# Optimization experiments

Measured on AMD Instinct MI355X. Metric: run time of the kernel, lower is better.

Reference implementation:

```python
import jax, jax.numpy as jnp
import numpy as np

N_NODES = 500_000
N_EDGES = 8_000_000
N_GRAPHS = 1000


def _mlp(x, w1, b1, w2, b2):
    # Linear -> SELU -> Linear (torch Sequential equivalent)
    return jax.nn.selu(x @ w1 + b1) @ w2 + b2


def setup_inputs() -> dict:
    key = jax.random.key(0)
    ks = jax.random.split(key, 25)
    p = lambda i, shape: jax.random.normal(ks[i], shape, jnp.float32) * 0.1
    return {
        "nodes": jax.random.normal(ks[0], (N_NODES, 1), jnp.float32),
        "edges": jax.random.normal(ks[1], (N_EDGES, 1), jnp.float32),
        "senders": jax.random.randint(ks[2], (N_EDGES,), 0, N_NODES),
        "receivers": jax.random.randint(ks[3], (N_EDGES,), 0, N_NODES),
        "graph_ids": jnp.sort(jax.random.randint(ks[4], (N_NODES,), 0, N_GRAPHS)),
        "num_graphs": N_GRAPHS,
        # permutate_nodes: 2 -> 10 -> 10
        "pn_w1": p(5, (2, 10)), "pn_b1": p(6, (10,)), "pn_w2": p(7, (10, 10)), "pn_b2": p(8, (10,)),
        # update_edges: 11 -> 5 -> 1
        "ue_w1": p(9, (11, 5)), "ue_b1": p(10, (5,)), "ue_w2": p(11, (5, 1)), "ue_b2": p(12, (1,)),
        # permutate_edges: 1 -> 5 -> 10
        "pe_w1": p(13, (1, 5)), "pe_b1": p(14, (5,)), "pe_w2": p(15, (5, 10)), "pe_b2": p(16, (10,)),
        # update_nodes: 11 -> 5 -> 1
        "un_w1": p(17, (11, 5)), "un_b1": p(18, (5,)), "un_w2": p(19, (5, 1)), "un_b2": p(20, (1,)),
        # predict: 11 -> 10 -> 10
        "pr_w1": p(21, (11, 10)), "pr_b1": p(22, (10,)), "pr_w2": p(23, (10, 10)), "pr_b2": p(24, (10,)),
    }


def reference(nodes, edges, pn_w1, pn_b1, pn_w2, pn_b2,
              ue_w1, ue_b1, ue_w2, ue_b2,
              pe_w1, pe_b1, pe_w2, pe_b2,
              un_w1, un_b1, un_w2, un_b2,
              pr_w1, pr_b1, pr_w2, pr_b2,
              senders, receivers, graph_ids, num_graphs):
    # gather node feats to edges: [recv || send] -> (E, 2)
    collected = jnp.concatenate([nodes[receivers], nodes[senders]], axis=-1)
    h1_nodes = _mlp(collected, pn_w1, pn_b1, pn_w2, pn_b2)  # (E, 10)
    h1_edges = edges  # (E, 1)
    for _ in range(3):
        h1_edges = _mlp(jnp.concatenate([h1_edges, h1_nodes], axis=-1),
                        ue_w1, ue_b1, ue_w2, ue_b2)  # (E, 1)
    # edges -> nodes aggregation (sum over receiver)
    edges_of_nodes = jax.ops.segment_sum(h1_edges, receivers, num_segments=nodes.shape[0])  # (N, 1)
    h2_edges = _mlp(edges_of_nodes, pe_w1, pe_b1, pe_w2, pe_b2)  # (N, 10)
    h2_nodes = nodes  # (N, 1)
    for _ in range(3):
        h2_nodes = _mlp(jnp.concatenate([h2_nodes, h2_edges], axis=-1),
                        un_w1, un_b1, un_w2, un_b2)  # (N, 1)
    # nodes -> globals aggregation (sum per graph)
    g = jax.ops.segment_sum(jnp.concatenate([h2_nodes, h2_edges], axis=-1),
                            graph_ids, num_segments=num_graphs)  # (G, 11)
    out = _mlp(g, pr_w1, pr_b1, pr_w2, pr_b2)  # (G, 10)
    return jax.nn.softmax(out, axis=-1)
```

## Files before the change

### kernel.cpp

```cpp
#include <hip/hip_runtime.h>
#include <hip/hip_fp16.h>
#include <math.h>

#define N_NODES_C  500000
#define N_EDGES_C  8000000
#define N_GRAPHS_C 1000
#define NGROUPS_C  (N_EDGES_C / 4)

#define BSHIFT  11
#define BWIDTH  2048
#define NBKT    245
#define PART_TPB 512
#define EPB     16384
#define GPB     (EPB / 4)
#define NPB     ((NGROUPS_C + GPB - 1) / GPB)
#define SROW    496
#define RITER   (GPB / PART_TPB)

#define G_BSHIFT 10
#define G_BWIDTH 1024
#define G_NBKT   489
#define P3_TPB  512
#define EPB3    8192
#define GPB3    (EPB3 / 4)
#define NPB3    ((NGROUPS_C + GPB3 - 1) / GPB3)
#define RITER3  (GPB3 / P3_TPB)

#define GRAPH_ACC_OFF 0
#define PARTIALS_OFF  11008
#define FW_OFF        33024
#define ZERO_HEAD     33024

#define STARTS_OFF    33280
#define PAIRS_OFF     (STARTS_OFF + 246 * SROW)
#define WS_WORDS_NEEDED (PAIRS_OFF + NPB * EPB)

#define GTOT_OFF   33248
#define GCUR_OFF   33760
#define RPFX_OFF   34272
#define PAIRS3_OFF 34784
#define WS3_WORDS_NEEDED (PAIRS3_OFF + N_EDGES_C * 2)

#define OLD_NODE_ACC_OFF 33536
#define OLD_ZERO_WORDS   (OLD_NODE_ACC_OFF + N_NODES_C)

#define LOG2E_F 1.4426950408889634f


__device__ __forceinline__ float selu2(float xl) {
    const float C1 = 0.7282901039f;
    const float C2 = 1.7580993408473766f;
    float e = __builtin_amdgcn_exp2f(xl);
    float neg = fmaf(C2, e, -C2);
    return xl > 0.0f ? C1 * xl : neg;
}

__device__ __forceinline__ float selu_f(float x) {
    const float scale = 1.0507009873554805f;
    const float sa    = 1.0507009873554805f * 1.6732632423543772f;
    float neg = sa * (__expf(x) - 1.0f);
    return x > 0.0f ? scale * x : neg;
}

__device__ __forceinline__ void atomAddF(float* p, float v) {
    __hip_atomic_fetch_add(p, v, __ATOMIC_RELAXED, __HIP_MEMORY_SCOPE_AGENT);
}

__device__ __forceinline__ void fuse_weights(
        int t,
        const float* __restrict__ pn_w1, const float* __restrict__ pn_b1,
        const float* __restrict__ pn_w2, const float* __restrict__ pn_b2,
        const float* __restrict__ ue_w1, const float* __restrict__ ue_b1,
        const float* __restrict__ ue_w2, const float* __restrict__ ue_b2,
        const float* __restrict__ pe_w1, const float* __restrict__ pe_b1,
        const float* __restrict__ pe_w2, const float* __restrict__ pe_b2,
        const float* __restrict__ un_w1, const float* __restrict__ un_b1,
        const float* __restrict__ un_w2, const float* __restrict__ un_b2,
        float* __restrict__ fw) {
    const float L = LOG2E_F;
    if (t < 20) fw[0 + t] = pn_w1[t] * L;
    if (t < 10) fw[20 + t] = pn_b1[t] * L;
    if (t < 50) {
        int j = t / 5, k = t % 5;
        float s = 0.0f;
        for (int m = 0; m < 10; ++m) s += pn_w2[j * 10 + m] * ue_w1[(1 + m) * 5 + k];
        fw[30 + t] = s * L;
    }
    if (t < 5) {
        float s = ue_b1[t];
        for (int m = 0; m < 10; ++m) s += pn_b2[m] * ue_w1[(1 + m) * 5 + t];
        fw[80 + t] = s * L;
    }
    if (t < 5)  fw[85 + t]  = ue_w1[t] * L;
    if (t < 5)  fw[90 + t]  = ue_w2[t];
    if (t == 0) fw[95]      = ue_b2[0];
    if (t < 5)  fw[96 + t]  = pe_w1[t] * L;
    if (t < 5)  fw[101 + t] = pe_b1[t] * L;
    if (t < 50) fw[106 + t] = pe_w2[t];
    if (t < 10) fw[156 + t] = pe_b2[t];
    if (t < 25) {
        int j = t / 5, k = t % 5;
        float s = 0.0f;
        for (int m = 0; m < 10; ++m) s += pe_w2[j * 10 + m] * un_w1[(1 + m) * 5 + k];
        fw[166 + t] = s * L;
    }
    if (t < 5) {
        float s = un_b1[t];
        for (int m = 0; m < 10; ++m) s += pe_b2[m] * un_w1[(1 + m) * 5 + t];
        fw[191 + t] = s * L;
    }
    if (t < 5)  fw[196 + t] = un_w1[t] * L;
    if (t < 5)  fw[201 + t] = un_w2[t];
    if (t == 0) fw[206]     = un_b2[0];
}

__global__ __launch_bounds__(256) void k_init(
        float* __restrict__ ws,
        const float* pn_w1, const float* pn_b1, const float* pn_w2, const float* pn_b2,
        const float* ue_w1, const float* ue_b1, const float* ue_w2, const float* ue_b2,
        const float* pe_w1, const float* pe_b1, const float* pe_w2, const float* pe_b2,
        const float* un_w1, const float* un_b1, const float* un_w2, const float* un_b2) {
    int i = blockIdx.x * 256 + threadIdx.x;
    if (i < ZERO_HEAD) ws[i] = 0.0f;
    int* gtot = (int*)ws + GTOT_OFF;
    if (i < 512) gtot[i] = 0;
    if (blockIdx.x == 0)
        fuse_weights(threadIdx.x, pn_w1, pn_b1, pn_w2, pn_b2, ue_w1, ue_b1, ue_w2, ue_b2,
                     pe_w1, pe_b1, pe_w2, pe_b2, un_w1, un_b1, un_w2, un_b2, ws + FW_OFF);
}

__global__ void k_fuse(const float* pn_w1, const float* pn_b1, const float* pn_w2, const float* pn_b2,
                       const float* ue_w1, const float* ue_b1, const float* ue_w2, const float* ue_b2,
                       const float* pe_w1, const float* pe_b1, const float* pe_w2, const float* pe_b2,
                       const float* un_w1, const float* un_b1, const float* un_w2, const float* un_b2,
                       float* fw) {
    fuse_weights(threadIdx.x, pn_w1, pn_b1, pn_w2, pn_b2, ue_w1, ue_b1, ue_w2, ue_b2,
                 pe_w1, pe_b1, pe_w2, pe_b2, un_w1, un_b1, un_w2, un_b2, fw);
}

__global__ void k_final(const float* __restrict__ graph_acc,
                        const float* __restrict__ partials,
                        const float* __restrict__ pr_w1, const float* __restrict__ pr_b1,
                        const float* __restrict__ pr_w2, const float* __restrict__ pr_b2,
                        float* __restrict__ out) {
    int g = blockIdx.x * blockDim.x + threadIdx.x;
    if (g >= N_GRAPHS_C) return;
    float gv[11];
#pragma unroll
    for (int f = 0; f < 11; ++f)
        gv[f] = graph_acc[g * 11 + f] + partials[g * 11 + f] + partials[11000 + g * 11 + f];
    float h[10];
#pragma unroll
    for (int j = 0; j < 10; ++j) {
        float z = pr_b1[j];
#pragma unroll
        for (int f = 0; f < 11; ++f) z = fmaf(gv[f], pr_w1[f * 10 + j], z);
        h[j] = selu_f(z);
    }
    float o[10];
    float mx = -1e30f;
#pragma unroll
    for (int j = 0; j < 10; ++j) {
        float z = pr_b2[j];
#pragma unroll
        for (int m = 0; m < 10; ++m) z = fmaf(h[m], pr_w2[m * 10 + j], z);
        o[j] = z;
        mx = fmaxf(mx, z);
    }
    float sum = 0.0f;
#pragma unroll
    for (int j = 0; j < 10; ++j) { o[j] = __expf(o[j] - mx); sum += o[j]; }
    float inv = 1.0f / sum;
#pragma unroll
    for (int j = 0; j < 10; ++j) out[g * 10 + j] = o[j] * inv;
}


__global__ __launch_bounds__(P3_TPB) void k_hist(
        const int* __restrict__ receivers, int* __restrict__ gtot) {
    __shared__ int hist[512];
    int tid = threadIdx.x, p = blockIdx.x;
    int gstart = p * GPB3;
    int gnum   = NGROUPS_C - gstart;
    if (gnum > GPB3) gnum = GPB3;
    hist[tid] = 0;
    __syncthreads();
#pragma unroll
    for (int r = 0; r < RITER3; ++r) {
        int idx = r * P3_TPB + tid;
        int gi  = gstart + (idx < gnum ? idx : 0);
        int4 rv = ((const int4*)receivers)[gi];
        if (idx < gnum) {
            atomicAdd(&hist[rv.x >> G_BSHIFT], 1);
            atomicAdd(&hist[rv.y >> G_BSHIFT], 1);
            atomicAdd(&hist[rv.z >> G_BSHIFT], 1);
            atomicAdd(&hist[rv.w >> G_BSHIFT], 1);
        }
    }
    __syncthreads();
    int h = hist[tid];
    if (h) atomicAdd(&gtot[tid], h);
}

__global__ __launch_bounds__(512) void k_rowscan(
        const int* __restrict__ gtot, int* __restrict__ gcursor,
        int* __restrict__ rowprefix) {
    __shared__ int sc[512];
    int tid = threadIdx.x;
    int v = (tid < G_NBKT) ? gtot[tid] : 0;
    sc[tid] = v;
    __syncthreads();
    int val = v;
    for (int d = 1; d < 512; d <<= 1) {
        int add = (tid >= d) ? sc[tid - d] : 0;
        __syncthreads();
        if (tid >= d) { val += add; sc[tid] = val; }
        __syncthreads();
    }
    int excl = val - v;
    gcursor[tid]  = excl;
    rowprefix[tid] = excl;
    if (tid == G_NBKT - 1) rowprefix[G_NBKT] = val;
}

__global__ __launch_bounds__(P3_TPB, 4) void k_part3(
        const float* __restrict__ edges,
        const int* __restrict__ senders, const int* __restrict__ receivers,
        int* __restrict__ gcursor, unsigned long long* __restrict__ pairs64) {
    __shared__ int hist[512];
    __shared__ int cursor[512];
    __shared__ int lstartS[512];
    __shared__ int segbase[512];
    __shared__ alignas(16) unsigned long long staged[EPB3];

    int tid = threadIdx.x, p = blockIdx.x;
    int gstart = p * GPB3;
    int gnum   = NGROUPS_C - gstart;
    if (gnum > GPB3) gnum = GPB3;
    int E = gnum * 4;

    hist[tid] = 0;
    __syncthreads();

    int4 rv4[RITER3];
#pragma unroll
    for (int r = 0; r < RITER3; ++r) {
        int idx = r * P3_TPB + tid;
        int gi  = gstart + (idx < gnum ? idx : 0);
        rv4[r] = ((const int4*)receivers)[gi];
        if (idx < gnum) {
            atomicAdd(&hist[rv4[r].x >> G_BSHIFT], 1);
            atomicAdd(&hist[rv4[r].y >> G_BSHIFT], 1);
            atomicAdd(&hist[rv4[r].z >> G_BSHIFT], 1);
            atomicAdd(&hist[rv4[r].w >> G_BSHIFT], 1);
        }
    }
    __syncthreads();

    int orig = hist[tid], val = orig;
    for (int d = 1; d < 512; d <<= 1) {
        int add = (tid >= d) ? hist[tid - d] : 0;
        __syncthreads();
        if (tid >= d) { val += add; hist[tid] = val; }
        __syncthreads();
    }
    int excl = val - orig;
    cursor[tid]  = excl;
    lstartS[tid] = excl;
    __syncthreads();

    if (tid < G_NBKT) {
        int cnt = ((tid + 1 < 512) ? lstartS[tid + 1] : E) - excl;
        segbase[tid] = atomicAdd(&gcursor[tid], cnt);
    }

#pragma unroll
    for (int r = 0; r < RITER3; ++r) {
        int idx = r * P3_TPB + tid;
        int gi  = gstart + (idx < gnum ? idx : 0);
        float4 e4 = ((const float4*)edges)[gi];
        int4   s4 = ((const int4*)senders)[gi];
        int4   rv = rv4[r];
        if (idx < gnum) {
            int   rvv[4] = {rv.x, rv.y, rv.z, rv.w};
            int   svv[4] = {s4.x, s4.y, s4.z, s4.w};
            float evv[4] = {e4.x, e4.y, e4.z, e4.w};
#pragma unroll
            for (int u = 0; u < 4; ++u) {
                int bkt  = rvv[u] >> G_BSHIFT;
                int slot = atomicAdd(&cursor[bkt], 1);
                unsigned long long pk =
                    ((unsigned long long)(rvv[u] & (G_BWIDTH - 1)) << 51)
                  | ((unsigned long long)(unsigned)svv[u] << 32)
                  | (unsigned long long)__float_as_uint(evv[u]);
                staged[slot] = pk;
            }
        }
    }
    __syncthreads();

#pragma unroll 2
    for (int i = tid; i < E; i += P3_TPB) {
        int lo = 0, hi = 512;
#pragma unroll
        for (int s = 0; s < 9; ++s) {
            int mid = (lo + hi) >> 1;
            if (lstartS[mid] <= i) lo = mid; else hi = mid;
        }
        pairs64[(size_t)segbase[lo] + (i - lstartS[lo])] = staged[i];
    }
}

__global__ __launch_bounds__(1024, 8) void k_gather3(
        const float* __restrict__ nodes, const int* __restrict__ graph_ids,
        const float* __restrict__ fw, const int* __restrict__ rowprefix,
        const unsigned long long* __restrict__ pairs64,
        float* __restrict__ graph_acc, float* __restrict__ partials) {
    __shared__ float accf[G_BWIDTH];
    __shared__ float nf[G_BWIDTH];
    __shared__ float garr[32 * 11];
    int tid = threadIdx.x;
    int b   = blockIdx.x;

    int nodeBase = b << G_BSHIFT;
    int lastIdx  = nodeBase + G_BWIDTH;
    if (lastIdx > N_NODES_C) lastIdx = N_NODES_C;
    int lim = lastIdx - nodeBase;

    accf[tid] = 0.0f;
    nf[tid]   = (tid < lim) ? nodes[nodeBase + tid] : 0.0f;
    if (tid < 352) garr[tid] = 0.0f;
    int base = rowprefix[b];
    int end  = rowprefix[b + 1];
    __syncthreads();

    {
        float w_pn1[20], b_pn1[10], W_eb[50], b_eb[5], w1r0[5], w2e[5];
#pragma unroll
        for (int j = 0; j < 20; ++j) w_pn1[j] = fw[j];
#pragma unroll
        for (int j = 0; j < 10; ++j) b_pn1[j] = fw[20 + j];
#pragma unroll
        for (int j = 0; j < 50; ++j) W_eb[j] = fw[30 + j];
#pragma unroll
        for (int j = 0; j < 5; ++j) b_eb[j] = fw[80 + j];
#pragma unroll
        for (int j = 0; j < 5; ++j) w1r0[j] = fw[85 + j];
#pragma unroll
        for (int j = 0; j < 5; ++j) w2e[j] = fw[90 + j];
        float b2e = fw[95];

        int i = base + tid;
#pragma unroll 1
        for (; i + 1024 < end; i += 2048) {
            unsigned long long pkA = pairs64[i];
            unsigned long long pkB = pairs64[i + 1024];
            float nsA = nodes[(int)((pkA >> 32) & 0x7FFFFULL)];
            float nsB = nodes[(int)((pkB >> 32) & 0x7FFFFULL)];
            int   rlA = (int)(pkA >> 51);
            int   rlB = (int)(pkB >> 51);
            float nrA = nf[rlA];
            float nrB = nf[rlB];
            float eA  = __uint_as_float((unsigned)pkA);
            float eB  = __uint_as_float((unsigned)pkB);

            float bsA[5], bsB[5];
#pragma unroll
            for (int k = 0; k < 5; ++k) { bsA[k] = b_eb[k]; bsB[k] = b_eb[k]; }
#pragma unroll
            for (int j = 0; j < 10; ++j) {
                float zlA = fmaf(nrA, w_pn1[j], fmaf(nsA, w_pn1[10 + j], b_pn1[j]));
                float zlB = fmaf(nrB, w_pn1[j], fmaf(nsB, w_pn1[10 + j], b_pn1[j]));
                float szA = selu2(zlA);
                float szB = selu2(zlB);
#pragma unroll
                for (int k = 0; k < 5; ++k) {
                    bsA[k] = fmaf(szA, W_eb[j * 5 + k], bsA[k]);
                    bsB[k] = fmaf(szB, W_eb[j * 5 + k], bsB[k]);
                }
            }
#pragma unroll
            for (int it = 0; it < 3; ++it) {
                float aA = b2e, aB = b2e;
#pragma unroll
                for (int k = 0; k < 5; ++k) {
                    float tA = selu2(fmaf(eA, w1r0[k], bsA[k]));
                    float tB = selu2(fmaf(eB, w1r0[k], bsB[k]));
                    aA = fmaf(tA, w2e[k], aA);
                    aB = fmaf(tB, w2e[k], aB);
                }
                eA = aA; eB = aB;
            }
            atomicAdd(&accf[rlA], eA);
            atomicAdd(&accf[rlB], eB);
        }
#pragma unroll 1
        for (; i < end; i += 1024) {
            unsigned long long pk = pairs64[i];
            int   rl   = (int)(pk >> 51);
            int   sidx = (int)((pk >> 32) & 0x7FFFFULL);
            float e    = __uint_as_float((unsigned)pk);
            float nr   = nf[rl];
            float ns   = nodes[sidx];

            float bs[5];
#pragma unroll
            for (int k = 0; k < 5; ++k) bs[k] = b_eb[k];
#pragma unroll
            for (int j = 0; j < 10; ++j) {
                float zl = fmaf(nr, w_pn1[j], fmaf(ns, w_pn1[10 + j], b_pn1[j]));
                float sz = selu2(zl);
#pragma unroll
                for (int k = 0; k < 5; ++k) bs[k] = fmaf(sz, W_eb[j * 5 + k], bs[k]);
            }
#pragma unroll
            for (int it = 0; it < 3; ++it) {
                float acc2 = b2e;
#pragma unroll
                for (int k = 0; k < 5; ++k) {
                    float tt = selu2(fmaf(e, w1r0[k], bs[k]));
                    acc2 = fmaf(tt, w2e[k], acc2);
                }
                e = acc2;
            }
            atomicAdd(&accf[rl], e);
        }
    }
    __syncthreads();

    float w_pe1[5], b_pe1[5], pe_w2[50], pe_b2[10], W_nb[25], b_nb[5], w1r0n[5], w2n[5];
#pragma unroll
    for (int j = 0; j < 5; ++j) w_pe1[j] = fw[96 + j];
#pragma unroll
    for (int j = 0; j < 5; ++j) b_pe1[j] = fw[101 + j];
#pragma unroll
    for (int j = 0; j < 50; ++j) pe_w2[j] = fw[106 + j];
#pragma unroll
    for (int j = 0; j < 10; ++j) pe_b2[j] = fw[156 + j];
#pragma unroll
    for (int j = 0; j < 25; ++j) W_nb[j] = fw[166 + j];
#pragma unroll
    for (int j = 0; j < 5; ++j) b_nb[j] = fw[191 + j];
#pragma unroll
    for (int j = 0; j < 5; ++j) w1r0n[j] = fw[196 + j];
#pragma unroll
    for (int j = 0; j < 5; ++j) w2n[j] = fw[201 + j];
    float b2n = fw[206];

    int gidBase = graph_ids[nodeBase];
    int gidEnd  = graph_ids[lastIdx - 1];

    {
        int i = nodeBase + tid;
        bool valid = tid < lim;

        float s = accf[tid];
        float t5[5];
#pragma unroll
        for (int k = 0; k < 5; ++k) t5[k] = selu2(fmaf(s, w_pe1[k], b_pe1[k]));
        float he[10];
#pragma unroll
        for (int m = 0; m < 10; ++m) {
            float a = pe_b2[m];
#pragma unroll
            for (int k = 0; k < 5; ++k) a = fmaf(t5[k], pe_w2[k * 10 + m], a);
            he[m] = a;
        }
        float bs[5];
#pragma unroll
        for (int k = 0; k < 5; ++k) {
            float a = b_nb[k];
#pragma unroll
            for (int t = 0; t < 5; ++t) a = fmaf(t5[t], W_nb[t * 5 + k], a);
            bs[k] = a;
        }
        float n = valid ? nf[tid] : 0.0f;
#pragma unroll
        for (int it = 0; it < 3; ++it) {
            float a = b2n;
#pragma unroll
            for (int k = 0; k < 5; ++k) {
                float tt = selu2(fmaf(n, w1r0n[k], bs[k]));
                a = fmaf(tt, w2n[k], a);
            }
            n = a;
        }

        int gid = valid ? graph_ids[i] : -1;
        if (!valid) {
            n = 0.0f;
#pragma unroll
            for (int m = 0; m < 10; ++m) he[m] = 0.0f;
        }

        int gid0 = __shfl(gid, 0, 64);
        bool allsame = __all(gid == gid0) && (gid0 >= 0);
        if (allsame) {
            float vv = n;
#pragma unroll
            for (int off = 32; off > 0; off >>= 1) vv += __shfl_down(vv, off, 64);
            float vh[10];
#pragma unroll
            for (int m = 0; m < 10; ++m) {
                float ww = he[m];
#pragma unroll
                for (int off = 32; off > 0; off >>= 1) ww += __shfl_down(ww, off, 64);
                vh[m] = ww;
            }
            if ((tid & 63) == 0) {
                int off = gid0 - gidBase;
                if (off >= 0 && off < 32) {
                    atomicAdd(&garr[off * 11 + 0], vv);
#pragma unroll
                    for (int m = 0; m < 10; ++m) atomicAdd(&garr[off * 11 + 1 + m], vh[m]);
                } else {
                    atomAddF(&graph_acc[gid0 * 11 + 0], vv);
#pragma unroll
                    for (int m = 0; m < 10; ++m) atomAddF(&graph_acc[gid0 * 11 + 1 + m], vh[m]);
                }
            }
        } else if (valid) {
            int off = gid - gidBase;
            if (off >= 0 && off < 32) {
                atomicAdd(&garr[off * 11 + 0], n);
#pragma unroll
                for (int m = 0; m < 10; ++m) atomicAdd(&garr[off * 11 + 1 + m], he[m]);
            } else {
                atomAddF(&graph_acc[gid * 11 + 0], n);
#pragma unroll
                for (int m = 0; m < 10; ++m) atomAddF(&graph_acc[gid * 11 + 1 + m], he[m]);
            }
        }
    }
    __syncthreads();

    int ngl = gidEnd - gidBase + 1;
    if (ngl > 32) ngl = 32;
    int par = (b & 1) * 11000;
    for (int t = tid; t < ngl * 11; t += 1024) {
        int off = t / 11, f = t - off * 11;
        partials[par + (gidBase + off) * 11 + f] = garr[t];
    }
}


__global__ __launch_bounds__(PART_TPB, 4) void k_part(
        const float* __restrict__ nodes, const float* __restrict__ edges,
        const int* __restrict__ senders, const int* __restrict__ receivers,
        const float* __restrict__ fw, int* __restrict__ starts_T,
        unsigned int* __restrict__ pairs) {
    __shared__ int hist[256];
    __shared__ int cursorS[256];
    __shared__ unsigned int staged[EPB];

    int tid = threadIdx.x;
    int p   = blockIdx.x;
    int gstart = p * GPB;
    int gnum   = NGROUPS_C - gstart;
    if (gnum > GPB) gnum = GPB;

    float w_pn1[20], b_pn1[10], W_eb[50], b_eb[5], w1r0[5], w2e[5];
#pragma unroll
    for (int j = 0; j < 20; ++j) w_pn1[j] = fw[j];
#pragma unroll
    for (int j = 0; j < 10; ++j) b_pn1[j] = fw[20 + j];
#pragma unroll
    for (int j = 0; j < 50; ++j) W_eb[j] = fw[30 + j];
#pragma unroll
    for (int j = 0; j < 5; ++j) b_eb[j] = fw[80 + j];
#pragma unroll
    for (int j = 0; j < 5; ++j) w1r0[j] = fw[85 + j];
#pragma unroll
    for (int j = 0; j < 5; ++j) w2e[j] = fw[90 + j];
    float b2e = fw[95];

    if (tid < 256) hist[tid] = 0;
    __syncthreads();

#pragma unroll 1
    for (int r = 0; r < RITER; ++r) {
        int idx = r * PART_TPB + tid;
        int gi  = gstart + (idx < gnum ? idx : 0);
        int4 rv = ((const int4*)receivers)[gi];
        if (idx < gnum) {
            atomicAdd(&hist[rv.x >> BSHIFT], 1);
            atomicAdd(&hist[rv.y >> BSHIFT], 1);
            atomicAdd(&hist[rv.z >> BSHIFT], 1);
            atomicAdd(&hist[rv.w >> BSHIFT], 1);
        }
    }
    __syncthreads();

    int orig = 0, val = 0;
    if (tid < 256) { orig = hist[tid]; val = orig; }
    for (int d = 1; d < 256; d <<= 1) {
        int add = 0;
        if (tid >= d && tid < 256) add = hist[tid - d];
        __syncthreads();
        if (tid >= d && tid < 256) { val += add; hist[tid] = val; }
        __syncthreads();
    }
    int excl = val - orig;
    if (tid < 256) cursorS[tid] = excl;
    if (tid < 246) starts_T[tid * SROW + p] = excl;
    __syncthreads();

    float4 e4A, e4B, e4N;
    int4   s4A, s4B, s4N, r4A, r4B, r4N;
    float  nsA0, nsA1, nsA2, nsA3, nrA0, nrA1, nrA2, nrA3;
    float  nsB0, nsB1, nsB2, nsB3, nrB0, nrB1, nrB2, nrB3;

    {
        int gi0 = gstart + (tid < gnum ? tid : 0);
        e4A = ((const float4*)edges)[gi0];
        s4A = ((const int4*)senders)[gi0];
        r4A = ((const int4*)receivers)[gi0];
        nsA0 = nodes[s4A.x]; nsA1 = nodes[s4A.y];
        nsA2 = nodes[s4A.z]; nsA3 = nodes[s4A.w];
        nrA0 = nodes[r4A.x]; nrA1 = nodes[r4A.y];
        nrA2 = nodes[r4A.z]; nrA3 = nodes[r4A.w];
        int idx1 = PART_TPB + tid;
        int gi1 = gstart + (idx1 < gnum ? idx1 : 0);
        e4B = ((const float4*)edges)[gi1];
        s4B = ((const int4*)senders)[gi1];
        r4B = ((const int4*)receivers)[gi1];
    }

#pragma unroll 1
    for (int r = 0; r < RITER; ++r) {
        {
            int idx2 = (r + 2) * PART_TPB + tid;
            int gi2  = gstart + (idx2 < gnum ? idx2 : 0);
            e4N = ((const float4*)edges)[gi2];
            s4N = ((const int4*)senders)[gi2];
            r4N = ((const int4*)receivers)[gi2];
        }
        nsB0 = nodes[s4B.x]; nsB1 = nodes[s4B.y];
        nsB2 = nodes[s4B.z]; nsB3 = nodes[s4B.w];
        nrB0 = nodes[r4B.x]; nrB1 = nodes[r4B.y];
        nrB2 = nodes[r4B.z]; nrB3 = nodes[r4B.w];

        float ev[4]  = {e4A.x, e4A.y, e4A.z, e4A.w};
        int   rv[4]  = {r4A.x, r4A.y, r4A.z, r4A.w};
        float nsv[4] = {nsA0, nsA1, nsA2, nsA3};
        float nrv[4] = {nrA0, nrA1, nrA2, nrA3};

        bool validr = (r * PART_TPB + tid) < gnum;
#pragma unroll
        for (int u = 0; u < 4; ++u) {
            float nr = nrv[u], ns = nsv[u];
            float bs[5];
#pragma unroll
            for (int k = 0; k < 5; ++k) bs[k] = b_eb[k];
#pragma unroll
            for (int j = 0; j < 10; ++j) {
                float zl = fmaf(nr, w_pn1[j], fmaf(ns, w_pn1[10 + j], b_pn1[j]));
                float sz = selu2(zl);
#pragma unroll
                for (int k = 0; k < 5; ++k) bs[k] = fmaf(sz, W_eb[j * 5 + k], bs[k]);
            }
            float e = ev[u];
#pragma unroll
            for (int it = 0; it < 3; ++it) {
                float acc2 = b2e;
#pragma unroll
                for (int k = 0; k < 5; ++k) {
                    float tt = selu2(fmaf(e, w1r0[k], bs[k]));
                    acc2 = fmaf(tt, w2e[k], acc2);
                }
                e = acc2;
            }
            if (validr) {
                int bkt  = rv[u] >> BSHIFT;
                int slot = atomicAdd(&cursorS[bkt], 1);
                unsigned int pk = ((unsigned int)(rv[u] & (BWIDTH - 1)) << 16)
                                | (unsigned int)__half_as_ushort(__float2half_rn(e));
                staged[slot] = pk;
            }
        }

        e4A = e4B; s4A = s4B; r4A = r4B;
        nsA0 = nsB0; nsA1 = nsB1; nsA2 = nsB2; nsA3 = nsB3;
        nrA0 = nrB0; nrA1 = nrB1; nrA2 = nrB2; nrA3 = nrB3;
        e4B = e4N; s4B = s4N; r4B = r4N;
    }
    __syncthreads();

    const uint4* staged4 = (const uint4*)staged;
    uint4* dst = (uint4*)(pairs + (size_t)p * EPB);
    for (int i = tid; i < gnum; i += PART_TPB) dst[i] = staged4[i];
}

__global__ __launch_bounds__(1024) void k_gather(
        const float* __restrict__ nodes, const int* __restrict__ graph_ids,
        const float* __restrict__ fw, const int* __restrict__ starts_T,
        const unsigned int* __restrict__ pairs, float* __restrict__ graph_acc,
        float* __restrict__ partials) {
    __shared__ float accf[BWIDTH];
    __shared__ int s0[SROW], s1[SROW];
    __shared__ float garr[32 * 11];
    int tid = threadIdx.x;
    int b   = blockIdx.x;

    accf[tid] = 0.0f; accf[1024 + tid] = 0.0f;
    if (tid < 352) garr[tid] = 0.0f;
    for (int i = tid; i < NPB; i += 1024) {
        s0[i] = starts_T[b * SROW + i];
        s1[i] = starts_T[(b + 1) * SROW + i];
    }
    __syncthreads();

    int g32 = tid >> 5, lane = tid & 31;
    for (int p = g32; p < NPB; p += 32) {
        int st = s0[p], en = s1[p];
        const unsigned int* seg = pairs + (size_t)p * EPB + st;
        int cnt = en - st;
        for (int i = lane; i < cnt; i += 32) {
            unsigned int pk = seg[i];
            atomicAdd(&accf[(pk >> 16) & (BWIDTH - 1)],
                      __half2float(__ushort_as_half((unsigned short)(pk & 0xffff))));
        }
    }
    __syncthreads();

    float w_pe1[5], b_pe1[5], pe_w2[50], pe_b2[10], W_nb[25], b_nb[5], w1r0n[5], w2n[5];
#pragma unroll
    for (int j = 0; j < 5; ++j) w_pe1[j] = fw[96 + j];
#pragma unroll
    for (int j = 0; j < 5; ++j) b_pe1[j] = fw[101 + j];
#pragma unroll
    for (int j = 0; j < 50; ++j) pe_w2[j] = fw[106 + j];
#pragma unroll
    for (int j = 0; j < 10; ++j) pe_b2[j] = fw[156 + j];
#pragma unroll
    for (int j = 0; j < 25; ++j) W_nb[j] = fw[166 + j];
#pragma unroll
    for (int j = 0; j < 5; ++j) b_nb[j] = fw[191 + j];
#pragma unroll
    for (int j = 0; j < 5; ++j) w1r0n[j] = fw[196 + j];
#pragma unroll
    for (int j = 0; j < 5; ++j) w2n[j] = fw[201 + j];
    float b2n = fw[206];

    int nodeBase = b << BSHIFT;
    int lastIdx  = nodeBase + BWIDTH;
    if (lastIdx > N_NODES_C) lastIdx = N_NODES_C;
    int gidBase = graph_ids[nodeBase];
    int gidEnd  = graph_ids[lastIdx - 1];

#pragma unroll
    for (int q = 0; q < 2; ++q) {
        int local = q * 1024 + tid;
        int i = nodeBase + local;
        bool valid = i < N_NODES_C;

        float s = accf[local];
        float t5[5];
#pragma unroll
        for (int k = 0; k < 5; ++k) t5[k] = selu2(fmaf(s, w_pe1[k], b_pe1[k]));
        float he[10];
#pragma unroll
        for (int m = 0; m < 10; ++m) {
            float a = pe_b2[m];
#pragma unroll
            for (int k = 0; k < 5; ++k) a = fmaf(t5[k], pe_w2[k * 10 + m], a);
            he[m] = a;
        }
        float bs[5];
#pragma unroll
        for (int k = 0; k < 5; ++k) {
            float a = b_nb[k];
#pragma unroll
            for (int t = 0; t < 5; ++t) a = fmaf(t5[t], W_nb[t * 5 + k], a);
            bs[k] = a;
        }
        float n = valid ? nodes[i] : 0.0f;
#pragma unroll
        for (int it = 0; it < 3; ++it) {
            float a = b2n;
#pragma unroll
            for (int k = 0; k < 5; ++k) {
                float tt = selu2(fmaf(n, w1r0n[k], bs[k]));
                a = fmaf(tt, w2n[k], a);
            }
            n = a;
        }

        int gid = valid ? graph_ids[i] : -1;
        if (!valid) {
            n = 0.0f;
#pragma unroll
            for (int m = 0; m < 10; ++m) he[m] = 0.0f;
        }

        int gid0 = __shfl(gid, 0, 64);
        bool allsame = __all(gid == gid0) && (gid0 >= 0);
        if (allsame) {
            float v = n;
#pragma unroll
            for (int off = 32; off > 0; off >>= 1) v += __shfl_down(v, off, 64);
            float vh[10];
#pragma unroll
            for (int m = 0; m < 10; ++m) {
                float ww = he[m];
#pragma unroll
                for (int off = 32; off > 0; off >>= 1) ww += __shfl_down(ww, off, 64);
                vh[m] = ww;
            }
            if ((tid & 63) == 0) {
                int off = gid0 - gidBase;
                if (off >= 0 && off < 32) {
                    atomicAdd(&garr[off * 11 + 0], v);
#pragma unroll
                    for (int m = 0; m < 10; ++m) atomicAdd(&garr[off * 11 + 1 + m], vh[m]);
                } else {
                    atomAddF(&graph_acc[gid0 * 11 + 0], v);
#pragma unroll
                    for (int m = 0; m < 10; ++m) atomAddF(&graph_acc[gid0 * 11 + 1 + m], vh[m]);
                }
            }
        } else if (valid) {
            int off = gid - gidBase;
            if (off >= 0 && off < 32) {
                atomicAdd(&garr[off * 11 + 0], n);
#pragma unroll
                for (int m = 0; m < 10; ++m) atomicAdd(&garr[off * 11 + 1 + m], he[m]);
            } else {
                atomAddF(&graph_acc[gid * 11 + 0], n);
#pragma unroll
                for (int m = 0; m < 10; ++m) atomAddF(&graph_acc[gid * 11 + 1 + m], he[m]);
            }
        }
    }
    __syncthreads();

    int ngl = gidEnd - gidBase + 1;
    if (ngl > 32) ngl = 32;
    int par = (b & 1) * 11000;
    for (int t = tid; t < ngl * 11; t += 1024) {
        int off = t / 11, f = t - off * 11;
        partials[par + (gidBase + off) * 11 + f] = garr[t];
    }
}


__global__ __launch_bounds__(256) void k_zero(float* __restrict__ ws, int len4) {
    int i = blockIdx.x * 256 + threadIdx.x;
    if (i < len4) ((float4*)ws)[i] = make_float4(0.f, 0.f, 0.f, 0.f);
}

__global__ __launch_bounds__(256) void k_edges(
        const float* __restrict__ nodes, const float* __restrict__ edges,
        const int* __restrict__ senders, const int* __restrict__ receivers,
        const float* __restrict__ fw, float* __restrict__ node_acc) {
    float w_pn1[20], b_pn1[10], W_eb[50], b_eb[5], w1r0[5], w2e[5];
#pragma unroll
    for (int j = 0; j < 20; ++j) w_pn1[j] = fw[j];
#pragma unroll
    for (int j = 0; j < 10; ++j) b_pn1[j] = fw[20 + j];
#pragma unroll
    for (int j = 0; j < 50; ++j) W_eb[j] = fw[30 + j];
#pragma unroll
    for (int j = 0; j < 5; ++j) b_eb[j] = fw[80 + j];
#pragma unroll
    for (int j = 0; j < 5; ++j) w1r0[j] = fw[85 + j];
#pragma unroll
    for (int j = 0; j < 5; ++j) w2e[j] = fw[90 + j];
    float b2e = fw[95];

    int g = blockIdx.x * 256 + threadIdx.x;
    if (g >= NGROUPS_C) return;

    float4 e4 = ((const float4*)edges)[g];
    int4  s4 = ((const int4*)senders)[g];
    int4  r4 = ((const int4*)receivers)[g];
    float ev[4] = {e4.x, e4.y, e4.z, e4.w};
    int   sv[4] = {s4.x, s4.y, s4.z, s4.w};
    int   rv[4] = {r4.x, r4.y, r4.z, r4.w};
    float nsv[4], nrv[4];
#pragma unroll
    for (int u = 0; u < 4; ++u) { nsv[u] = nodes[sv[u]]; nrv[u] = nodes[rv[u]]; }
#pragma unroll
    for (int u = 0; u < 4; ++u) {
        float nr = nrv[u], ns = nsv[u];
        float bs[5];
#pragma unroll
        for (int k = 0; k < 5; ++k) bs[k] = b_eb[k];
#pragma unroll
        for (int j = 0; j < 10; ++j) {
            float zl = fmaf(nr, w_pn1[j], fmaf(ns, w_pn1[10 + j], b_pn1[j]));
            float sz = selu2(zl);
#pragma unroll
            for (int k = 0; k < 5; ++k) bs[k] = fmaf(sz, W_eb[j * 5 + k], bs[k]);
        }
        float e = ev[u];
#pragma unroll
        for (int it = 0; it < 3; ++it) {
            float acc2 = b2e;
#pragma unroll
            for (int k = 0; k < 5; ++k) {
                float tt = selu2(fmaf(e, w1r0[k], bs[k]));
                acc2 = fmaf(tt, w2e[k], acc2);
            }
            e = acc2;
        }
        atomAddF(&node_acc[rv[u]], e);
    }
}

__global__ __launch_bounds__(256) void k_nodes(
        const float* __restrict__ nodes, const int* __restrict__ graph_ids,
        const float* __restrict__ fw, const float* __restrict__ node_acc,
        float* __restrict__ graph_acc) {
    float w_pe1[5], b_pe1[5], pe_w2[50], pe_b2[10], W_nb[25], b_nb[5], w1r0n[5], w2n[5];
#pragma unroll
    for (int j = 0; j < 5; ++j) w_pe1[j] = fw[96 + j];
#pragma unroll
    for (int j = 0; j < 5; ++j) b_pe1[j] = fw[101 + j];
#pragma unroll
    for (int j = 0; j < 50; ++j) pe_w2[j] = fw[106 + j];
#pragma unroll
    for (int j = 0; j < 10; ++j) pe_b2[j] = fw[156 + j];
#pragma unroll
    for (int j = 0; j < 25; ++j) W_nb[j] = fw[166 + j];
#pragma unroll
    for (int j = 0; j < 5; ++j) b_nb[j] = fw[191 + j];
#pragma unroll
    for (int j = 0; j < 5; ++j) w1r0n[j] = fw[196 + j];
#pragma unroll
    for (int j = 0; j < 5; ++j) w2n[j] = fw[201 + j];
    float b2n = fw[206];

    int i = blockIdx.x * 256 + threadIdx.x;
    bool valid = i < N_NODES_C;
    int ii = valid ? i : (N_NODES_C - 1);

    float s = node_acc[ii];
    float t5[5];
#pragma unroll
    for (int k = 0; k < 5; ++k) t5[k] = selu2(fmaf(s, w_pe1[k], b_pe1[k]));
    float he[10];
#pragma unroll
    for (int m = 0; m < 10; ++m) {
        float a = pe_b2[m];
#pragma unroll
        for (int k = 0; k < 5; ++k) a = fmaf(t5[k], pe_w2[k * 10 + m], a);
        he[m] = a;
    }
    float bs[5];
#pragma unroll
    for (int k = 0; k < 5; ++k) {
        float a = b_nb[k];
#pragma unroll
        for (int t = 0; t < 5; ++t) a = fmaf(t5[t], W_nb[t * 5 + k], a);
        bs[k] = a;
    }
    float n = nodes[ii];
#pragma unroll
    for (int it = 0; it < 3; ++it) {
        float a = b2n;
#pragma unroll
        for (int k = 0; k < 5; ++k) {
            float tt = selu2(fmaf(n, w1r0n[k], bs[k]));
            a = fmaf(tt, w2n[k], a);
        }
        n = a;
    }

    int gid = valid ? graph_ids[ii] : -1;
    if (!valid) {
        n = 0.0f;
#pragma unroll
        for (int m = 0; m < 10; ++m) he[m] = 0.0f;
    }

    int gid0 = __shfl(gid, 0, 64);
    bool allsame = __all(gid == gid0) && (gid0 >= 0);
    if (allsame) {
        float v = n;
#pragma unroll
        for (int off = 32; off > 0; off >>= 1) v += __shfl_down(v, off, 64);
        float vh[10];
#pragma unroll
        for (int m = 0; m < 10; ++m) {
            float ww = he[m];
#pragma unroll
            for (int off = 32; off > 0; off >>= 1) ww += __shfl_down(ww, off, 64);
            vh[m] = ww;
        }
        if ((threadIdx.x & 63) == 0) {
            atomAddF(&graph_acc[gid0 * 11 + 0], v);
#pragma unroll
            for (int m = 0; m < 10; ++m) atomAddF(&graph_acc[gid0 * 11 + 1 + m], vh[m]);
        }
    } else if (valid) {
        atomAddF(&graph_acc[gid * 11 + 0], n);
#pragma unroll
        for (int m = 0; m < 10; ++m) atomAddF(&graph_acc[gid * 11 + 1 + m], he[m]);
    }
}


extern "C" void kernel_launch(void* const* d_in, const int* in_sizes, int n_in,
                              void* d_out, int out_size, void* d_ws, size_t ws_size,
                              hipStream_t stream) {
    const float* nodes     = (const float*)d_in[0];
    const float* edges     = (const float*)d_in[1];
    const int*   senders   = (const int*)d_in[2];
    const int*   receivers = (const int*)d_in[3];
    const int*   graph_ids = (const int*)d_in[4];
    const float* pn_w1 = (const float*)d_in[6];
    const float* pn_b1 = (const float*)d_in[7];
    const float* pn_w2 = (const float*)d_in[8];
    const float* pn_b2 = (const float*)d_in[9];
    const float* ue_w1 = (const float*)d_in[10];
    const float* ue_b1 = (const float*)d_in[11];
    const float* ue_w2 = (const float*)d_in[12];
    const float* ue_b2 = (const float*)d_in[13];
    const float* pe_w1 = (const float*)d_in[14];
    const float* pe_b1 = (const float*)d_in[15];
    const float* pe_w2 = (const float*)d_in[16];
    const float* pe_b2 = (const float*)d_in[17];
    const float* un_w1 = (const float*)d_in[18];
    const float* un_b1 = (const float*)d_in[19];
    const float* un_w2 = (const float*)d_in[20];
    const float* un_b2 = (const float*)d_in[21];
    const float* pr_w1 = (const float*)d_in[22];
    const float* pr_b1 = (const float*)d_in[23];
    const float* pr_w2 = (const float*)d_in[24];
    const float* pr_b2 = (const float*)d_in[25];

    float* ws        = (float*)d_ws;
    float* graph_acc = ws + GRAPH_ACC_OFF;
    float* partials  = ws + PARTIALS_OFF;
    float* fw        = ws + FW_OFF;
    float* outp      = (float*)d_out;

    if (ws_size >= (size_t)WS3_WORDS_NEEDED * 4) {
        int* gtot      = (int*)ws + GTOT_OFF;
        int* gcursor   = (int*)ws + GCUR_OFF;
        int* rowprefix = (int*)ws + RPFX_OFF;
        unsigned long long* pairs64 = (unsigned long long*)((int*)ws + PAIRS3_OFF);

        hipLaunchKernelGGL(k_init, dim3((ZERO_HEAD + 255) / 256), dim3(256), 0, stream, ws,
                           pn_w1, pn_b1, pn_w2, pn_b2, ue_w1, ue_b1, ue_w2, ue_b2,
                           pe_w1, pe_b1, pe_w2, pe_b2, un_w1, un_b1, un_w2, un_b2);
        hipLaunchKernelGGL(k_hist, dim3(NPB3), dim3(P3_TPB), 0, stream,
                           receivers, gtot);
        hipLaunchKernelGGL(k_rowscan, dim3(1), dim3(512), 0, stream,
                           gtot, gcursor, rowprefix);
        hipLaunchKernelGGL(k_part3, dim3(NPB3), dim3(P3_TPB), 0, stream,
                           edges, senders, receivers, gcursor, pairs64);
        hipLaunchKernelGGL(k_gather3, dim3(G_NBKT), dim3(1024), 0, stream,
                           nodes, graph_ids, fw, rowprefix, pairs64, graph_acc, partials);
        hipLaunchKernelGGL(k_final, dim3((N_GRAPHS_C + 255) / 256), dim3(256), 0, stream,
                           graph_acc, partials, pr_w1, pr_b1, pr_w2, pr_b2, outp);
    } else if (ws_size >= (size_t)WS_WORDS_NEEDED * 4) {
        int* starts_T        = (int*)ws + STARTS_OFF;
        unsigned int* pairs  = (unsigned int*)ws + PAIRS_OFF;

        hipLaunchKernelGGL(k_init, dim3((ZERO_HEAD + 255) / 256), dim3(256), 0, stream, ws,
                           pn_w1, pn_b1, pn_w2, pn_b2, ue_w1, ue_b1, ue_w2, ue_b2,
                           pe_w1, pe_b1, pe_w2, pe_b2, un_w1, un_b1, un_w2, un_b2);
        hipLaunchKernelGGL(k_part, dim3(NPB), dim3(PART_TPB), 0, stream,
                           nodes, edges, senders, receivers, fw, starts_T, pairs);
        hipLaunchKernelGGL(k_gather, dim3(NBKT), dim3(1024), 0, stream,
                           nodes, graph_ids, fw, starts_T, pairs, graph_acc, partials);
        hipLaunchKernelGGL(k_final, dim3((N_GRAPHS_C + 255) / 256), dim3(256), 0, stream,
                           graph_acc, partials, pr_w1, pr_b1, pr_w2, pr_b2, outp);
    } else {
        float* node_acc = ws + OLD_NODE_ACC_OFF;
        int len4 = OLD_ZERO_WORDS / 4;
        hipLaunchKernelGGL(k_zero, dim3((len4 + 255) / 256), dim3(256), 0, stream, ws, len4);
        hipLaunchKernelGGL(k_fuse, dim3(1), dim3(64), 0, stream,
                           pn_w1, pn_b1, pn_w2, pn_b2, ue_w1, ue_b1, ue_w2, ue_b2,
                           pe_w1, pe_b1, pe_w2, pe_b2, un_w1, un_b1, un_w2, un_b2, fw);
        hipLaunchKernelGGL(k_edges, dim3((NGROUPS_C + 255) / 256), dim3(256), 0, stream,
                           nodes, edges, senders, receivers, fw, node_acc);
        hipLaunchKernelGGL(k_nodes, dim3((N_NODES_C + 255) / 256), dim3(256), 0, stream,
                           nodes, graph_ids, fw, node_acc, graph_acc);
        hipLaunchKernelGGL(k_final, dim3((N_GRAPHS_C + 255) / 256), dim3(256), 0, stream,
                           graph_acc, partials, pr_w1, pr_b1, pr_w2, pr_b2, outp);
    }
}
```

Before: 338.0 us.

## Pre-gather sender node values in partition pass and pack edges as fp16

The partition kernel now loads senders early, gathers nodes[sender] there, and packs that float value into the 64-bit pair along with an fp16 edge value and a 16-bit local receiver index. The gather kernel no longer does a dependent random load of nodes. The init work is fused into the histogram kernel, with gtot cleared by a memset. Nontemporal loads and stores are used for the streaming data, and the part3 occupancy hint is lowered. Rounding the edge feature to fp16 adds numerical error.

Result: slower. 372.7 us (+10.2%).

```diff
diff --git a/kernel.cpp b/kernel.cpp
--- a/kernel.cpp
+++ b/kernel.cpp
@@ -45,6 +45,9 @@
 #define OLD_ZERO_WORDS   (OLD_NODE_ACC_OFF + N_NODES_C)
 
 #define LOG2E_F 1.4426950408889634f
+
+typedef int   int4v __attribute__((ext_vector_type(4)));
+typedef float flt4v __attribute__((ext_vector_type(4)));
 
 
 __device__ __forceinline__ float selu2(float xl) {
@@ -122,8 +125,6 @@
         const float* un_w1, const float* un_b1, const float* un_w2, const float* un_b2) {
     int i = blockIdx.x * 256 + threadIdx.x;
     if (i < ZERO_HEAD) ws[i] = 0.0f;
-    int* gtot = (int*)ws + GTOT_OFF;
-    if (i < 512) gtot[i] = 0;
     if (blockIdx.x == 0)
         fuse_weights(threadIdx.x, pn_w1, pn_b1, pn_w2, pn_b2, ue_w1, ue_b1, ue_w2, ue_b2,
                      pe_w1, pe_b1, pe_w2, pe_b2, un_w1, un_b1, un_w2, un_b2, ws + FW_OFF);
@@ -176,10 +177,21 @@
 }
 
 
-__global__ __launch_bounds__(P3_TPB) void k_hist(
-        const int* __restrict__ receivers, int* __restrict__ gtot) {
+__global__ __launch_bounds__(P3_TPB) void k_inithist(
+        float* __restrict__ ws, const int* __restrict__ receivers,
+        int* __restrict__ gtot,
+        const float* pn_w1, const float* pn_b1, const float* pn_w2, const float* pn_b2,
+        const float* ue_w1, const float* ue_b1, const float* ue_w2, const float* ue_b2,
+        const float* pe_w1, const float* pe_b1, const float* pe_w2, const float* pe_b2,
+        const float* un_w1, const float* un_b1, const float* un_w2, const float* un_b2) {
     __shared__ int hist[512];
     int tid = threadIdx.x, p = blockIdx.x;
+    int gt = p * P3_TPB + tid;
+    if (gt < ZERO_HEAD) ws[gt] = 0.0f;
+    if (p == 0)
+        fuse_weights(tid, pn_w1, pn_b1, pn_w2, pn_b2, ue_w1, ue_b1, ue_w2, ue_b2,
+                     pe_w1, pe_b1, pe_w2, pe_b2, un_w1, un_b1, un_w2, un_b2, ws + FW_OFF);
+
     int gstart = p * GPB3;
     int gnum   = NGROUPS_C - gstart;
     if (gnum > GPB3) gnum = GPB3;
@@ -189,12 +201,12 @@
     for (int r = 0; r < RITER3; ++r) {
         int idx = r * P3_TPB + tid;
         int gi  = gstart + (idx < gnum ? idx : 0);
-        int4 rv = ((const int4*)receivers)[gi];
+        int4v rv = __builtin_nontemporal_load((const int4v*)receivers + gi);
         if (idx < gnum) {
-            atomicAdd(&hist[rv.x >> G_BSHIFT], 1);
-            atomicAdd(&hist[rv.y >> G_BSHIFT], 1);
-            atomicAdd(&hist[rv.z >> G_BSHIFT], 1);
-            atomicAdd(&hist[rv.w >> G_BSHIFT], 1);
+            atomicAdd(&hist[rv[0] >> G_BSHIFT], 1);
+            atomicAdd(&hist[rv[1] >> G_BSHIFT], 1);
+            atomicAdd(&hist[rv[2] >> G_BSHIFT], 1);
+            atomicAdd(&hist[rv[3] >> G_BSHIFT], 1);
         }
     }
     __syncthreads();
@@ -223,8 +235,8 @@
     if (tid == G_NBKT - 1) rowprefix[G_NBKT] = val;
 }
 
-__global__ __launch_bounds__(P3_TPB, 4) void k_part3(
-        const float* __restrict__ edges,
+__global__ __launch_bounds__(P3_TPB, 2) void k_part3(
+        const float* __restrict__ nodes, const float* __restrict__ edges,
         const int* __restrict__ senders, const int* __restrict__ receivers,
         int* __restrict__ gcursor, unsigned long long* __restrict__ pairs64) {
     __shared__ int hist[512];
@@ -242,17 +254,19 @@
     hist[tid] = 0;
     __syncthreads();
 
-    int4 rv4[RITER3];
+    int4v rv4[RITER3];
+    int4v s4v[RITER3];
 #pragma unroll
     for (int r = 0; r < RITER3; ++r) {
         int idx = r * P3_TPB + tid;
         int gi  = gstart + (idx < gnum ? idx : 0);
-        rv4[r] = ((const int4*)receivers)[gi];
+        rv4[r] = __builtin_nontemporal_load((const int4v*)receivers + gi);
+        s4v[r] = __builtin_nontemporal_load((const int4v*)senders + gi);
         if (idx < gnum) {
-            atomicAdd(&hist[rv4[r].x >> G_BSHIFT], 1);
-            atomicAdd(&hist[rv4[r].y >> G_BSHIFT], 1);
-            atomicAdd(&hist[rv4[r].z >> G_BSHIFT], 1);
-            atomicAdd(&hist[rv4[r].w >> G_BSHIFT], 1);
+            atomicAdd(&hist[rv4[r][0] >> G_BSHIFT], 1);
+            atomicAdd(&hist[rv4[r][1] >> G_BSHIFT], 1);
+            atomicAdd(&hist[rv4[r][2] >> G_BSHIFT], 1);
+            atomicAdd(&hist[rv4[r][3] >> G_BSHIFT], 1);
         }
     }
     __syncthreads();
@@ -274,25 +288,30 @@
         segbase[tid] = atomicAdd(&gcursor[tid], cnt);
     }
 
+    float nsv[RITER3][4];
+#pragma unroll
+    for (int r = 0; r < RITER3; ++r) {
+        nsv[r][0] = nodes[s4v[r][0]];
+        nsv[r][1] = nodes[s4v[r][1]];
+        nsv[r][2] = nodes[s4v[r][2]];
+        nsv[r][3] = nodes[s4v[r][3]];
+    }
+
 #pragma unroll
     for (int r = 0; r < RITER3; ++r) {
         int idx = r * P3_TPB + tid;
         int gi  = gstart + (idx < gnum ? idx : 0);
-        float4 e4 = ((const float4*)edges)[gi];
-        int4   s4 = ((const int4*)senders)[gi];
-        int4   rv = rv4[r];
+        flt4v e4 = __builtin_nontemporal_load((const flt4v*)edges + gi);
         if (idx < gnum) {
-            int   rvv[4] = {rv.x, rv.y, rv.z, rv.w};
-            int   svv[4] = {s4.x, s4.y, s4.z, s4.w};
-            float evv[4] = {e4.x, e4.y, e4.z, e4.w};
 #pragma unroll
             for (int u = 0; u < 4; ++u) {
-                int bkt  = rvv[u] >> G_BSHIFT;
+                int rv   = rv4[r][u];
+                int bkt  = rv >> G_BSHIFT;
                 int slot = atomicAdd(&cursor[bkt], 1);
                 unsigned long long pk =
-                    ((unsigned long long)(rvv[u] & (G_BWIDTH - 1)) << 51)
-                  | ((unsigned long long)(unsigned)svv[u] << 32)
-                  | (unsigned long long)__float_as_uint(evv[u]);
+                    ((unsigned long long)(rv & (G_BWIDTH - 1)) << 48)
+                  | ((unsigned long long)__half_as_ushort(__float2half_rn(e4[u])) << 32)
+                  | (unsigned long long)__float_as_uint(nsv[r][u]);
                 staged[slot] = pk;
             }
         }
@@ -307,7 +326,8 @@
             int mid = (lo + hi) >> 1;
             if (lstartS[mid] <= i) lo = mid; else hi = mid;
         }
-        pairs64[(size_t)segbase[lo] + (i - lstartS[lo])] = staged[i];
+        __builtin_nontemporal_store(
+            staged[i], &pairs64[(size_t)segbase[lo] + (i - lstartS[lo])]);
     }
 }
 
@@ -353,16 +373,16 @@
         int i = base + tid;
 #pragma unroll 1
         for (; i + 1024 < end; i += 2048) {
-            unsigned long long pkA = pairs64[i];
-            unsigned long long pkB = pairs64[i + 1024];
-            float nsA = nodes[(int)((pkA >> 32) & 0x7FFFFULL)];
-            float nsB = nodes[(int)((pkB >> 32) & 0x7FFFFULL)];
-            int   rlA = (int)(pkA >> 51);
-            int   rlB = (int)(pkB >> 51);
+            unsigned long long pkA = __builtin_nontemporal_load(&pairs64[i]);
+            unsigned long long pkB = __builtin_nontemporal_load(&pairs64[i + 1024]);
+            int   rlA = (int)(pkA >> 48);
+            int   rlB = (int)(pkB >> 48);
+            float eA  = __half2float(__ushort_as_half((unsigned short)(pkA >> 32)));
+            float eB  = __half2float(__ushort_as_half((unsigned short)(pkB >> 32)));
+            float nsA = __uint_as_float((unsigned)pkA);
+            float nsB = __uint_as_float((unsigned)pkB);
             float nrA = nf[rlA];
             float nrB = nf[rlB];
-            float eA  = __uint_as_float((unsigned)pkA);
-            float eB  = __uint_as_float((unsigned)pkB);
 
             float bsA[5], bsB[5];
 #pragma unroll
@@ -396,12 +416,11 @@
         }
 #pragma unroll 1
         for (; i < end; i += 1024) {
-            unsigned long long pk = pairs64[i];
-            int   rl   = (int)(pk >> 51);
-            int   sidx = (int)((pk >> 32) & 0x7FFFFULL);
-            float e    = __uint_as_float((unsigned)pk);
-            float nr   = nf[rl];
-            float ns   = nodes[sidx];
+            unsigned long long pk = __builtin_nontemporal_load(&pairs64[i]);
+            int   rl = (int)(pk >> 48);
+            float e  = __half2float(__ushort_as_half((unsigned short)(pk >> 32)));
+            float ns = __uint_as_float((unsigned)pk);
+            float nr = nf[rl];
 
             float bs[5];
 #pragma unroll
@@ -1042,15 +1061,15 @@
         int* rowprefix = (int*)ws + RPFX_OFF;
         unsigned long long* pairs64 = (unsigned long long*)((int*)ws + PAIRS3_OFF);
 
-        hipLaunchKernelGGL(k_init, dim3((ZERO_HEAD + 255) / 256), dim3(256), 0, stream, ws,
+        hipMemsetAsync(gtot, 0, 512 * sizeof(int), stream);
+        hipLaunchKernelGGL(k_inithist, dim3(NPB3), dim3(P3_TPB), 0, stream,
+                           ws, receivers, gtot,
                            pn_w1, pn_b1, pn_w2, pn_b2, ue_w1, ue_b1, ue_w2, ue_b2,
                            pe_w1, pe_b1, pe_w2, pe_b2, un_w1, un_b1, un_w2, un_b2);
-        hipLaunchKernelGGL(k_hist, dim3(NPB3), dim3(P3_TPB), 0, stream,
-                           receivers, gtot);
         hipLaunchKernelGGL(k_rowscan, dim3(1), dim3(512), 0, stream,
                            gtot, gcursor, rowprefix);
         hipLaunchKernelGGL(k_part3, dim3(NPB3), dim3(P3_TPB), 0, stream,
-                           edges, senders, receivers, gcursor, pairs64);
+                           nodes, edges, senders, receivers, gcursor, pairs64);
         hipLaunchKernelGGL(k_gather3, dim3(G_NBKT), dim3(1024), 0, stream,
                            nodes, graph_ids, fw, rowprefix, pairs64, graph_acc, partials);
         hipLaunchKernelGGL(k_final, dim3((N_GRAPHS_C + 255) / 256), dim3(256), 0, stream,
```
